# Kernel optimization log

Hardware: AMD Instinct MI355X
Metric: run time of the kernel (lower is better)

## Reference

```python
import jax, jax.numpy as jnp
import numpy as np
from jax import lax

B, N, T, H, E, V, F = 16, 5, 10, 512, 250, 30000, 2048  # N must be num_layers*num_dirs+1 = 5


def setup_inputs() -> dict:
    key = jax.random.key(0)
    ks = jax.random.split(key, 20)
    s = 0.05
    def rn(k, shp):
        return jax.random.normal(k, shp, jnp.float32) * s
    z = lambda n: jnp.zeros((n,), jnp.float32)
    return {
        "img": jax.random.normal(ks[0], (B, F), jnp.float32),
        "caps": jax.random.randint(ks[1], (B, N, T), 0, V, dtype=jnp.int32),
        "Wh1": rn(ks[2], (F, 2 * H)), "bh1": z(2 * H),
        "Wh2": rn(ks[3], (2 * H, H)), "bh2": z(H),
        "Wc1": rn(ks[4], (F, 2 * H)), "bc1": z(2 * H),
        "Wc2": rn(ks[5], (2 * H, H)), "bc2": z(H),
        "emb": rn(ks[6], (V, E)),
        "Wih0f": rn(ks[7], (E, 4 * H)), "Whh0f": rn(ks[8], (H, 4 * H)), "b0f": z(4 * H),
        "Wih0b": rn(ks[9], (E, 4 * H)), "Whh0b": rn(ks[10], (H, 4 * H)), "b0b": z(4 * H),
        "Wih1f": rn(ks[11], (2 * H, 4 * H)), "Whh1f": rn(ks[12], (H, 4 * H)), "b1f": z(4 * H),
        "Wih1b": rn(ks[13], (2 * H, 4 * H)), "Whh1b": rn(ks[14], (H, 4 * H)), "b1b": z(4 * H),
        "Wfc": rn(ks[15], (2 * H, V)), "bfc": z(V),
    }


def _lstm_dir(x, h0, c0, Wih, Whh, b, reverse):
    # x: [t, B, in]; PyTorch gate order i, f, g, o
    xs = x[::-1] if reverse else x
    xg = xs @ Wih + b  # precomputed input projection [t, B, 4H]
    def step(carry, xg_t):
        h, c = carry
        g = xg_t + h @ Whh
        i, f, gg, o = jnp.split(g, 4, axis=-1)
        c = jax.nn.sigmoid(f) * c + jax.nn.sigmoid(i) * jnp.tanh(gg)
        h = jax.nn.sigmoid(o) * jnp.tanh(c)
        return (h, c), h
    (hT, cT), hs = lax.scan(step, (h0, c0), xg)
    if reverse:
        hs = hs[::-1]
    return hs, hT, cT


def _bilstm2(x, h0, c0, p):
    # 2-layer bidirectional LSTM; state layout [l0_fwd, l0_bwd, l1_fwd, l1_bwd]
    of, hf0, cf0 = _lstm_dir(x, h0[0], c0[0], *p[0], False)
    ob, hb0, cb0 = _lstm_dir(x, h0[1], c0[1], *p[1], True)
    x1 = jnp.concatenate([of, ob], axis=-1)  # [t, B, 2H]
    o1f, hf1, cf1 = _lstm_dir(x1, h0[2], c0[2], *p[2], False)
    o1b, hb1, cb1 = _lstm_dir(x1, h0[3], c0[3], *p[3], True)
    out = jnp.concatenate([o1f, o1b], axis=-1)  # [t, B, 2H]
    hN = jnp.stack([hf0, hb0, hf1, hb1])
    cN = jnp.stack([cf0, cb0, cf1, cb1])
    return out, hN, cN


def _forward(img, caps, Wh1, bh1, Wh2, bh2, Wc1, bc1, Wc2, bc2, emb,
             Wih0f, Whh0f, b0f, Wih0b, Whh0b, b0b,
             Wih1f, Whh1f, b1f, Wih1b, Whh1b, b1b, Wfc, bfc):
    relu = jax.nn.relu
    h = relu(relu(img @ Wh1 + bh1) @ Wh2 + bh2)  # init_h MLP (dropout = identity in eval)
    c = relu(relu(img @ Wc1 + bc1) @ Wc2 + bc2)  # init_c MLP
    hs = jnp.broadcast_to(h[None], (N - 1, B, H))  # N-1 == 4 == num_layers*num_dirs
    cs = jnp.broadcast_to(c[None], (N - 1, B, H))
    seq = jnp.transpose(emb[caps], (1, 2, 0, 3))  # [N, T, B, E] caption-major prefixes
    p = ((Wih0f, Whh0f, b0f), (Wih0b, Whh0b, b0b),
         (Wih1f, Whh1f, b1f), (Wih1b, Whh1b, b1b))
    outs = None
    # Faithful reproduction of the original's redundant prefix recomputation:
    # at each outer step t, the LSTM is re-run on every caption's length-(t+1)
    # prefix, chaining (h, c) across captions; only the final step's outputs
    # survive, but the state chain depends on all prior iterations.
    for t in range(T):
        outs_t = []
        for n in range(N):
            o, hs, cs = _bilstm2(seq[n, :t + 1], hs, cs, p)
            outs_t.append(o)
        outs = outs_t
    out = jnp.stack(outs)  # [N, T, B, 2H]
    return out @ Wfc + bfc  # logits [N, T, B, V]


def reference(img, caps, Wh1, bh1, Wh2, bh2, Wc1, bc1, Wc2, bc2, emb,
              Wih0f, Whh0f, b0f, Wih0b, Whh0b, b0b,
              Wih1f, Whh1f, b1f, Wih1b, Whh1b, b1b, Wfc, bfc):
    return _forward(img, caps, Wh1, bh1, Wh2, bh2, Wc1, bc1, Wc2, bc2, emb,
                    Wih0f, Whh0f, b0f, Wih0b, Whh0b, b0b,
                    Wih1f, Whh1f, b1f, Wih1b, Whh1b, b1b, Wfc, bfc)
```

## Files before the change

kernel.cpp:

```cpp
#include <hip/hip_runtime.h>

typedef unsigned short u16;
typedef unsigned int   u32;
typedef unsigned long long u64;
typedef __attribute__((ext_vector_type(8))) short s8v;
typedef __attribute__((ext_vector_type(4))) float f4v;

#define DEVI __device__ __forceinline__

#define B_  16
#define N_  5
#define T_  10
#define H_  512
#define E_  250
#define V_  30000
#define F_  2048
#define FH  2048
#define H2  1024
#define NCOMP 128

__device__ u32   g_flag;
__device__ u32   g_slot[NCOMP];
__device__ __attribute__((aligned(64))) u16   g_H0[4*2*16*512];
__device__ __attribute__((aligned(64))) u16   g_H1[4*2*16*512];
__device__ __attribute__((aligned(64))) float g_cinit[16*512];
__device__ __attribute__((aligned(64))) u16   g_A1[2*2*16*1024];
__device__ __attribute__((aligned(64))) u16   g_X1[2*2*10*16*1024];
__device__ __attribute__((aligned(64))) u16   g_OUT1[2*800*1024];
__device__ __attribute__((aligned(64))) u16   g_TOK[800*256];

DEVI f4v MFMA(s8v a, s8v b, f4v c){ return __builtin_amdgcn_mfma_f32_16x16x32_bf16(a,b,c,0,0,0); }
DEVI float bf2f(u16 u){ union{u32 i; float f;} v; v.i = ((u32)u)<<16; return v.f; }
DEVI u16 f2bf(float f){ union{float f; u32 i;} v; v.f = f; u32 i = v.i + 0x7fffu + ((v.i>>16)&1u); return (u16)(i>>16); }
DEVI float sigm(float x){ return 1.0f/(1.0f+__expf(-x)); }
DEVI float tanhfast(float x){ float e = __expf(2.0f*x); return 1.0f - 2.0f/(e+1.0f); }

DEVI s8v ld16(const u16* p){ return *(const s8v*)p; }
DEVI s8v ld16u(const u16* p){ s8v a; __builtin_memcpy(&a, p, 16); return a; }

DEVI void ldc(s8v& d, const u16* p){
  asm volatile("global_load_dwordx4 %0, %1, off sc0 sc1" : "=v"(d) : "v"(p));
}
template<int N> DEVI void waitv(s8v& a){
  asm volatile("s_waitcnt vmcnt(%1)" : "+v"(a) : "n"(N));
}
template<int N> DEVI void waitv2(s8v& a, s8v& b){
  asm volatile("s_waitcnt vmcnt(%2)" : "+v"(a), "+v"(b) : "n"(N));
}

DEVI void st2c(u16* p, u16 v){
  asm volatile("global_store_short %0, %1, off sc0 sc1" :: "v"(p), "v"((u32)v) : "memory");
}

DEVI u16 ldw(const void* W, size_t idx, int f32){
  return f32 ? f2bf(((const float*)W)[idx]) : ((const u16*)W)[idx];
}
DEVI float ldwf(const void* W, size_t idx, int f32){
  return f32 ? ((const float*)W)[idx] : bf2f(((const u16*)W)[idx]);
}
DEVI s8v ldA8(const void* A, size_t idx, int f32){
  if(f32){
    const float* p = (const float*)A + idx;
    s8v a;
    #pragma unroll
    for(int j=0;j<8;++j) a[j] = (short)f2bf(p[j]);
    return a;
  }
  return ld16u((const u16*)A + idx);
}
DEVI s8v gatherBf(const void* W, int ld, int row0, int col, int f32){
  s8v r;
  #pragma unroll
  for(int j=0;j<8;++j) r[j] = (short)ldw(W, (size_t)(row0+j)*ld + col, f32);
  return r;
}

#define RPT4(M,b)  M(b) M((b)+1) M((b)+2) M((b)+3)
#define RPT8(M,b)  RPT4(M,b) RPT4(M,(b)+4)
#define RPT16(M,b) RPT8(M,b) RPT8(M,(b)+8)

__global__ __launch_bounds__(64) void k0(const void* img){
  int l = threadIdx.x;
  const u16* p = (const u16*)img;
  int bad = 0;
  #pragma unroll
  for(int i=0;i<4;++i){
    float v = bf2f(p[l + 64*i]);
    if(!(fabsf(v) <= 1e4f)) bad = 1;
  }
  unsigned long long mb = __ballot(bad);
  g_slot[l] = 0u; g_slot[l+64] = 0u;
  if(l==0){ g_flag = (mb != 0ull) ? 1u : 0u; }
}

__global__ __launch_bounds__(256) void k_tok(const int* caps, const void* emb){
  int f32 = (int)g_flag;
  int idx = blockIdx.x*256 + threadIdx.x;
  int bnr = idx>>8, e = idx&255;
  int tok = caps[bnr];
  u16 v = (e < E_) ? ldw(emb, (size_t)tok*E_ + e, f32) : (u16)0;
  g_TOK[idx] = v;
}

__global__ __launch_bounds__(256) void k1a(const void* img, const void* Wh1, const void* bh1,
                                           const void* Wc1, const void* bc1){
  int f32 = (int)g_flag;
  int w = threadIdx.x>>6, l = threadIdx.x&63, q = l>>4, c = l&15, m = l&15;
  int widx = blockIdx.x*4 + w;
  int which = widx>>6;
  int ct    = widx&63;
  const void* W    = which? Wc1 : Wh1;
  const void* bias = which? bc1 : bh1;
  int col = ct*16 + c;
  f4v acc = {0.f,0.f,0.f,0.f};
  for(int kc=0; kc<64; ++kc){
    s8v a = ldA8(img, (size_t)m*F_ + kc*32 + q*8, f32);
    s8v b = gatherBf(W, H2, kc*32+q*8, col, f32);
    acc = MFMA(a,b,acc);
  }
  float bi = ldwf(bias, col, f32);
  #pragma unroll
  for(int r=0;r<4;++r){
    float v = fmaxf(acc[r]+bi, 0.f);
    u16 hi = f2bf(v); u16 lo = f2bf(v - bf2f(hi));
    int rowb = q*4+r;
    g_A1[(size_t)(which*2+0)*B_*H2 + (size_t)rowb*H2 + col] = hi;
    g_A1[(size_t)(which*2+1)*B_*H2 + (size_t)rowb*H2 + col] = lo;
  }
}

__global__ __launch_bounds__(256) void k1b(const void* Wh2, const void* bh2,
                                           const void* Wc2, const void* bc2){
  int f32 = (int)g_flag;
  int w = threadIdx.x>>6, l = threadIdx.x&63, q = l>>4, c = l&15, m = l&15;
  int widx = blockIdx.x*4 + w;
  int which = widx>>5;
  int ct    = widx&31;
  const void* W    = which? Wc2 : Wh2;
  const void* bias = which? bc2 : bh2;
  const u16* Ab    = g_A1 + (size_t)which*2*B_*H2;
  int col = ct*16 + c;
  f4v acc = {0.f,0.f,0.f,0.f};
  for(int kc=0; kc<32; ++kc){
    s8v ah = ld16(Ab + (size_t)m*H2 + kc*32 + q*8);
    s8v al = ld16(Ab + (size_t)B_*H2 + (size_t)m*H2 + kc*32 + q*8);
    s8v b  = gatherBf(W, H_, kc*32+q*8, col, f32);
    acc = MFMA(ah,b,acc);
    acc = MFMA(al,b,acc);
  }
  float bi = ldwf(bias, col, f32);
  #pragma unroll
  for(int r=0;r<4;++r){
    float v = fmaxf(acc[r]+bi, 0.f);
    int rowb = q*4+r;
    if(which==0){
      u16 hi = f2bf(v); u16 lo = f2bf(v - bf2f(hi));
      #pragma unroll
      for(int dir=0; dir<2; ++dir){
        size_t base = (size_t)(dir*2+0)*16384;
        g_H0[base + 0*8192 + rowb*512 + col] = hi;  g_H0[base + 1*8192 + rowb*512 + col] = lo;
        g_H1[base + 0*8192 + rowb*512 + col] = hi;  g_H1[base + 1*8192 + rowb*512 + col] = lo;
      }
    } else {
      g_cinit[(size_t)rowb*H_ + col] = v;
    }
  }
}

DEVI void flag_publish(u32 ep){
  asm volatile("s_waitcnt vmcnt(0)" ::: "memory");
  __syncthreads();
  if(threadIdx.x==0)
    __hip_atomic_store(&g_slot[blockIdx.x], ep, __ATOMIC_RELAXED, __HIP_MEMORY_SCOPE_SYSTEM);
}
DEVI void flag_poll(u32 ep){
  int l = threadIdx.x & 63;
  for(;;){
    u32 a = __hip_atomic_load(&g_slot[l],    __ATOMIC_RELAXED, __HIP_MEMORY_SCOPE_SYSTEM);
    u32 b = __hip_atomic_load(&g_slot[l+64], __ATOMIC_RELAXED, __HIP_MEMORY_SCOPE_SYSTEM);
    if(__all((int)(a>=ep && b>=ep))) break;
    __builtin_amdgcn_s_sleep(1);
  }
  asm volatile("s_waitcnt vmcnt(0)" ::: "memory");
}

DEVI float gate_combine(f4v acc, float& cs, int l){
  int base = (l & 48) | (l & 3);
  int sel  = (l >> 2) & 3;
  float G[4];
  #pragma unroll
  for(int gg=0; gg<4; ++gg){
    int src = base | (gg<<2);
    float a0 = __shfl(acc[0], src, 64);
    float a1 = __shfl(acc[1], src, 64);
    float a2 = __shfl(acc[2], src, 64);
    float a3 = __shfl(acc[3], src, 64);
    float x = (sel&1)? a1 : a0;
    float y = (sel&1)? a3 : a2;
    G[gg] = (sel&2)? y : x;
  }
  float iG = sigm(G[0]);
  float fG = sigm(G[1]);
  float gG = tanhfast(G[2]);
  float oG = sigm(G[3]);
  cs = fG*cs + iG*gG;
  return oG * tanhfast(cs);
}

__global__ __launch_bounds__(128) void k2(const void* Wih0f, const void* Whh0f, const void* b0f,
                                          const void* Wih0b, const void* Whh0b, const void* b0b,
                                          const void* Wih1f, const void* Whh1f, const void* b1f,
                                          const void* Wih1b, const void* Whh1b, const void* b1b){
  __shared__ u16 sw[2*24576];
  int tid = threadIdx.x;
  int blk = blockIdx.x;
  int f32 = (int)g_flag;
  int wv  = tid>>6;
  int l   = tid&63;
  int q = l>>4, c = l&15, m = l&15;
  int dir = blk>>6; int blkd = blk&63;
  int hb  = blkd*8;
  int gc0 = (c>>2)*512 + hb + (c&3);
  int gc1 = gc0 + 4;
  int bo  = q*4 + (c>>2);
  int hc0 = hb + (c&3), hc1 = hc0 + 4;

  const void* Wih0 = dir? Wih0b : Wih0f;
  const void* Whh0 = dir? Whh0b : Whh0f;
  const void* b0   = dir? b0b   : b0f;
  const void* Wih1 = dir? Wih1b : Wih1f;
  const void* Whh1 = dir? Whh1b : Whh1f;
  const void* b1   = dir? b1b   : b1f;

  for(int tt=0; tt<2; ++tt){
    int gb = hb + tt*4;
    for(int ii=tid; ii<24576; ii+=128){
      int kc=ii>>9, rem=ii&511, cc=rem>>5, qq=(rem>>3)&3, j=ii&7;
      int gc = (cc>>2)*512 + gb + (cc&3);
      int rowk = kc*32+qq*8+j;
      sw[tt*24576+ii] = (rowk < H2) ? ldw(Wih1, (size_t)rowk*FH + gc, f32)
                                    : ldw(Whh1, (size_t)(rowk-H2)*FH + gc, f32);
    }
  }

  s8v w0a[16], w0b[16], wxa[8], wxb[8];
  float cA0=0.f, cA1=0.f, biasA0=0.f, biasA1=0.f;
  float cB0=0.f, cB1=0.f, biasB0=0.f, biasB1=0.f;
  if(wv==0){
    #pragma unroll
    for(int kc=0;kc<16;++kc){
      #pragma unroll
      for(int j=0;j<8;++j){
        int rowk = kc*32+q*8+j;
        w0a[kc][j] = (short)ldw(Whh0, (size_t)rowk*FH + gc0, f32);
        w0b[kc][j] = (short)ldw(Whh0, (size_t)rowk*FH + gc1, f32);
      }
    }
    #pragma unroll
    for(int kc=0;kc<8;++kc){
      #pragma unroll
      for(int j=0;j<8;++j){
        int rowk = kc*32+q*8+j;
        wxa[kc][j] = (rowk<E_)? (short)ldw(Wih0, (size_t)rowk*FH + gc0, f32) : (short)0;
        wxb[kc][j] = (rowk<E_)? (short)ldw(Wih0, (size_t)rowk*FH + gc1, f32) : (short)0;
      }
    }
    biasA0 = ldwf(b0, gc0, f32); biasA1 = ldwf(b0, gc1, f32);
    cA0 = g_cinit[(size_t)bo*H_ + hc0]; cA1 = g_cinit[(size_t)bo*H_ + hc1];
  } else {
    biasB0 = ldwf(b1, gc0, f32); biasB1 = ldwf(b1, gc1, f32);
    cB0 = g_cinit[(size_t)bo*H_ + hc0]; cB1 = g_cinit[(size_t)bo*H_ + hc1];
  }
  __syncthreads();

  u32 ep = 0;
  int p0 = 0, p1 = 0;
  for(int k=0; k<=50; ++k){
    int Lk = (k<50) ? (k/5 + 1) : 10;
    int Lp = (k==0) ? 0 : ((k-1)/5 + 1);
    int n0 = k - (k/5)*5;
    int km = k-1;
    int n1 = (k>0) ? (km - (km/5)*5) : 0;
    for(int s=0; s<Lk; ++s){
      if(wv==0){
        if(k<50){
          int row = dir ? (Lk-1-s) : s;
          const u16* er = g_TOK + ((size_t)(m*N_ + n0)*T_ + row)*256;
          const u16* Hr = g_H0 + (size_t)(dir*2 + p0)*16384;
          f4v A0 = {biasA0,biasA0,biasA0,biasA0};
          f4v A1 = {biasA1,biasA1,biasA1,biasA1};
          #pragma unroll
          for(int kc=0;kc<8;++kc){
            s8v a = ld16(er + kc*32 + q*8);
            A0 = MFMA(a, wxa[kc], A0); A1 = MFMA(a, wxb[kc], A1);
          }
          flag_poll(ep);
          s8v hst[16];
#define H0ISS(f) ldc(hst[(f)], Hr + (((f)&1)?8192u:0u) + (size_t)m*H_ + (((f)>>1)*32) + q*8);
#define H0STEP(f) { \
          waitv<(((f)<16)?15:(31-(f)))>(hst[(f)&15]); \
          A0 = MFMA(hst[(f)&15], w0a[(f)>>1], A0); \
          A1 = MFMA(hst[(f)&15], w0b[(f)>>1], A1); \
          if((f)+16<32) ldc(hst[(f)&15], Hr + (((f)&1)?8192u:0u) + (size_t)m*H_ + (((((f)+16))>>1)*32) + q*8); }
          RPT16(H0ISS,0)
          RPT16(H0STEP,0) RPT16(H0STEP,16)
          float hn0 = gate_combine(A0, cA0, l);
          float hn1 = gate_combine(A1, cA1, l);
          u16 h0h=f2bf(hn0), h0l=f2bf(hn0 - bf2f(h0h));
          u16 h1h=f2bf(hn1), h1l=f2bf(hn1 - bf2f(h1h));
          u16* Hw = g_H0 + (size_t)(dir*2 + (p0^1))*16384;
          st2c(Hw + (size_t)bo*H_ + hc0, h0h); st2c(Hw + 8192 + (size_t)bo*H_ + hc0, h0l);
          st2c(Hw + (size_t)bo*H_ + hc1, h1h); st2c(Hw + 8192 + (size_t)bo*H_ + hc1, h1l);
          u16* Xw = g_X1 + (size_t)(k&1)*327680;
          size_t xr = ((size_t)row*16 + bo)*H2 + dir*H_;
          st2c(Xw + xr + hc0, h0h); st2c(Xw + 163840 + xr + hc0, h0l);
          st2c(Xw + xr + hc1, h1h); st2c(Xw + 163840 + xr + hc1, h1l);
          p0 ^= 1;
        }
      } else {
        if(k>0 && s<Lp){
          int row = dir ? (Lp-1-s) : s;
          const u16* Xr  = g_X1 + (size_t)(km&1)*327680 + ((size_t)row*16)*H2;
          const u16* Xr2 = Xr + 163840;
          const u16* Hr1 = g_H1 + (size_t)(dir*2 + p1)*16384;
          f4v A0 = {biasB0,biasB0,biasB0,biasB0};
          f4v A1 = {biasB1,biasB1,biasB1,biasB1};
          s8v sh[12], sl[12];
          if(s==0) flag_poll(ep);
#define XISS(kc) { ldc(sh[(kc)], Xr + (size_t)m*H2 + ((kc)*32) + q*8); \
                   ldc(sl[(kc)], Xr2 + (size_t)m*H2 + ((kc)*32) + q*8); }
#define XSTEP(kc) { \
          waitv2<(((kc)<20)?22:(62-2*(kc)))>(sh[(kc)%12], sl[(kc)%12]); \
          s8v bf0 = ld16(sw + (kc)*512 + c*32 + q*8); \
          s8v bf1 = ld16(sw + 24576 + (kc)*512 + c*32 + q*8); \
          A0 = MFMA(sh[(kc)%12], bf0, A0); A0 = MFMA(sl[(kc)%12], bf0, A0); \
          A1 = MFMA(sh[(kc)%12], bf1, A1); A1 = MFMA(sl[(kc)%12], bf1, A1); \
          if((kc)+12<32){ ldc(sh[(kc)%12], Xr + (size_t)m*H2 + (((kc)+12)*32) + q*8); \
                          ldc(sl[(kc)%12], Xr2 + (size_t)m*H2 + (((kc)+12)*32) + q*8); } }
          RPT8(XISS,0) RPT4(XISS,8)
          RPT16(XSTEP,0) RPT16(XSTEP,16)
          if(s>0) flag_poll(ep);
#define H1ISS(h) { ldc(sh[(h)], Hr1 + (size_t)m*H_ + ((h)*32) + q*8); \
                   ldc(sl[(h)], Hr1 + 8192 + (size_t)m*H_ + ((h)*32) + q*8); }
#define H1STEP(h) { \
          waitv2<(((h)<4)?22:(30-2*(h)))>(sh[(h)%12], sl[(h)%12]); \
          s8v bf0 = ld16(sw + (32+(h))*512 + c*32 + q*8); \
          s8v bf1 = ld16(sw + 24576 + (32+(h))*512 + c*32 + q*8); \
          A0 = MFMA(sh[(h)%12], bf0, A0); A0 = MFMA(sl[(h)%12], bf0, A0); \
          A1 = MFMA(sh[(h)%12], bf1, A1); A1 = MFMA(sl[(h)%12], bf1, A1); \
          if((h)+12<16){ ldc(sh[(h)%12], Hr1 + (size_t)m*H_ + (((h)+12)*32) + q*8); \
                         ldc(sl[(h)%12], Hr1 + 8192 + (size_t)m*H_ + (((h)+12)*32) + q*8); } }
          RPT8(H1ISS,0) RPT4(H1ISS,8)
          RPT16(H1STEP,0)
          float hn0 = gate_combine(A0, cB0, l);
          float hn1 = gate_combine(A1, cB1, l);
          u16 h0h=f2bf(hn0), h0l=f2bf(hn0 - bf2f(h0h));
          u16 h1h=f2bf(hn1), h1l=f2bf(hn1 - bf2f(h1h));
          u16* Hw = g_H1 + (size_t)(dir*2 + (p1^1))*16384;
          st2c(Hw + (size_t)bo*H_ + hc0, h0h); st2c(Hw + 8192 + (size_t)bo*H_ + hc0, h0l);
          st2c(Hw + (size_t)bo*H_ + hc1, h1h); st2c(Hw + 8192 + (size_t)bo*H_ + hc1, h1l);
          size_t orow = (size_t)(n1*10 + row)*16 + bo;
          st2c(g_OUT1 + orow*H2 + dir*H_ + hc0, h0h);
          st2c(g_OUT1 + (size_t)800*H2 + orow*H2 + dir*H_ + hc0, h0l);
          st2c(g_OUT1 + orow*H2 + dir*H_ + hc1, h1h);
          st2c(g_OUT1 + (size_t)800*H2 + orow*H2 + dir*H_ + hc1, h1l);
          p1 ^= 1;
        }
      }
      flag_publish(ep+1);
      ++ep;
    }
  }
}

__global__ __launch_bounds__(256,1) void k3(const void* Wfc, const void* bfc, void* out){
  int f32 = (int)g_flag;
  int w = threadIdx.x>>6, l = threadIdx.x&63, q = l>>4, c = l&15, m = l&15;
  int ct = blockIdx.x*4 + w;
  if(ct >= 1875) return;
  int col = ct*16 + c;
  s8v bfr[32];
  #pragma unroll
  for(int kc=0; kc<32; ++kc){
    #pragma unroll
    for(int j=0;j<8;++j) bfr[kc][j] = (short)ldw(Wfc, (size_t)(kc*32+q*8+j)*V_ + col, f32);
  }
  float bi = ldwf(bfc, col, f32);
  for(int rt=0; rt<50; ++rt){
    f4v acc = {0.f,0.f,0.f,0.f};
    const u16* Ah = g_OUT1 + (size_t)(rt*16 + m)*H2;
    const u16* Al = Ah + (size_t)800*H2;
    #pragma unroll
    for(int kc=0; kc<32; ++kc){
      acc = MFMA(ld16(Ah + kc*32 + q*8), bfr[kc], acc);
      acc = MFMA(ld16(Al + kc*32 + q*8), bfr[kc], acc);
    }
    if(f32){
      float* o = (float*)out;
      #pragma unroll
      for(int r=0;r<4;++r) o[(size_t)(rt*16 + q*4 + r)*V_ + col] = acc[r] + bi;
    } else {
      u16* o = (u16*)out;
      #pragma unroll
      for(int r=0;r<4;++r) o[(size_t)(rt*16 + q*4 + r)*V_ + col] = f2bf(acc[r] + bi);
    }
  }
}

extern "C" void kernel_launch(void* const* d_in, const int* in_sizes, int n_in,
                              void* d_out, int out_size, void* d_ws, size_t ws_size,
                              hipStream_t stream){
  (void)in_sizes; (void)n_in; (void)out_size; (void)d_ws; (void)ws_size;
  const void* img  = d_in[0];
  const int*  caps = (const int*)d_in[1];
  const void* Wh1=d_in[2],  *bh1=d_in[3];
  const void* Wh2=d_in[4],  *bh2=d_in[5];
  const void* Wc1=d_in[6],  *bc1=d_in[7];
  const void* Wc2=d_in[8],  *bc2=d_in[9];
  const void* emb=d_in[10];
  const void* Wih0f=d_in[11], *Whh0f=d_in[12], *b0f=d_in[13];
  const void* Wih0b=d_in[14], *Whh0b=d_in[15], *b0b=d_in[16];
  const void* Wih1f=d_in[17], *Whh1f=d_in[18], *b1f=d_in[19];
  const void* Wih1b=d_in[20], *Whh1b=d_in[21], *b1b=d_in[22];
  const void* Wfc=d_in[23],  *bfc=d_in[24];

  hipLaunchKernelGGL(k0,    dim3(1),     dim3(64),  0, stream, img);
  hipLaunchKernelGGL(k_tok, dim3(800),   dim3(256), 0, stream, caps, emb);
  hipLaunchKernelGGL(k1a,   dim3(32),    dim3(256), 0, stream, img, Wh1, bh1, Wc1, bc1);
  hipLaunchKernelGGL(k1b,   dim3(16),    dim3(256), 0, stream, Wh2, bh2, Wc2, bc2);
  hipLaunchKernelGGL(k2,    dim3(NCOMP), dim3(128), 0, stream,
                     Wih0f, Whh0f, b0f, Wih0b, Whh0b, b0b,
                     Wih1f, Whh1f, b1f, Wih1b, Whh1b, b1b);
  hipLaunchKernelGGL(k3,    dim3(469),   dim3(256), 0, stream, Wfc, bfc, d_out);
}
```

Baseline: 3.612 ms.

## Decouple layer-0 and layer-1 LSTM waves with separate per-layer progress flags

```diff
diff --git a/kernel.cpp b/kernel.cpp
--- a/kernel.cpp
+++ b/kernel.cpp
@@ -20,12 +20,13 @@
 #define NCOMP 128
 
 __device__ u32   g_flag;
-__device__ u32   g_slot[NCOMP];
+__device__ u32   g_slot0[NCOMP];
+__device__ u32   g_slot1[NCOMP];
 __device__ __attribute__((aligned(64))) u16   g_H0[4*2*16*512];
 __device__ __attribute__((aligned(64))) u16   g_H1[4*2*16*512];
 __device__ __attribute__((aligned(64))) float g_cinit[16*512];
 __device__ __attribute__((aligned(64))) u16   g_A1[2*2*16*1024];
-__device__ __attribute__((aligned(64))) u16   g_X1[2*2*10*16*1024];
+__device__ __attribute__((aligned(64))) u16   g_X1[4*2*10*16*1024];
 __device__ __attribute__((aligned(64))) u16   g_OUT1[2*800*1024];
 __device__ __attribute__((aligned(64))) u16   g_TOK[800*256];
 
@@ -79,6 +80,31 @@
 #define RPT8(M,b)  RPT4(M,b) RPT4(M,(b)+4)
 #define RPT16(M,b) RPT8(M,b) RPT8(M,(b)+8)
 
+DEVI void publish_slot(u32* slot, u32 val){
+  asm volatile("s_waitcnt vmcnt(0)" ::: "memory");
+  if((threadIdx.x & 63)==0)
+    __hip_atomic_store(slot, val, __ATOMIC_RELAXED, __HIP_MEMORY_SCOPE_SYSTEM);
+}
+DEVI void poll_n64(u32* base, u32 tgt){
+  int l = threadIdx.x & 63;
+  for(;;){
+    u32 a = __hip_atomic_load(&base[l], __ATOMIC_RELAXED, __HIP_MEMORY_SCOPE_SYSTEM);
+    if(__all((int)(a>=tgt))) break;
+    __builtin_amdgcn_s_sleep(1);
+  }
+  asm volatile("s_waitcnt vmcnt(0)" ::: "memory");
+}
+DEVI void poll_n128(u32* base, u32 tgt){
+  int l = threadIdx.x & 63;
+  for(;;){
+    u32 a = __hip_atomic_load(&base[l],    __ATOMIC_RELAXED, __HIP_MEMORY_SCOPE_SYSTEM);
+    u32 b = __hip_atomic_load(&base[l+64], __ATOMIC_RELAXED, __HIP_MEMORY_SCOPE_SYSTEM);
+    if(__all((int)(a>=tgt && b>=tgt))) break;
+    __builtin_amdgcn_s_sleep(1);
+  }
+  asm volatile("s_waitcnt vmcnt(0)" ::: "memory");
+}
+
 __global__ __launch_bounds__(64) void k0(const void* img){
   int l = threadIdx.x;
   const u16* p = (const u16*)img;
@@ -89,7 +115,8 @@
     if(!(fabsf(v) <= 1e4f)) bad = 1;
   }
   unsigned long long mb = __ballot(bad);
-  g_slot[l] = 0u; g_slot[l+64] = 0u;
+  g_slot0[l] = 0u; g_slot0[l+64] = 0u;
+  g_slot1[l] = 0u; g_slot1[l+64] = 0u;
   if(l==0){ g_flag = (mb != 0ull) ? 1u : 0u; }
 }
 
@@ -167,23 +194,6 @@
   }
 }
 
-DEVI void flag_publish(u32 ep){
-  asm volatile("s_waitcnt vmcnt(0)" ::: "memory");
-  __syncthreads();
-  if(threadIdx.x==0)
-    __hip_atomic_store(&g_slot[blockIdx.x], ep, __ATOMIC_RELAXED, __HIP_MEMORY_SCOPE_SYSTEM);
-}
-DEVI void flag_poll(u32 ep){
-  int l = threadIdx.x & 63;
-  for(;;){
-    u32 a = __hip_atomic_load(&g_slot[l],    __ATOMIC_RELAXED, __HIP_MEMORY_SCOPE_SYSTEM);
-    u32 b = __hip_atomic_load(&g_slot[l+64], __ATOMIC_RELAXED, __HIP_MEMORY_SCOPE_SYSTEM);
-    if(__all((int)(a>=ep && b>=ep))) break;
-    __builtin_amdgcn_s_sleep(1);
-  }
-  asm volatile("s_waitcnt vmcnt(0)" ::: "memory");
-}
-
 DEVI float gate_combine(f4v acc, float& cs, int l){
   int base = (l & 48) | (l & 3);
   int sel  = (l >> 2) & 3;
@@ -273,102 +283,105 @@
   }
   __syncthreads();
 
-  u32 ep = 0;
-  int p0 = 0, p1 = 0;
-  for(int k=0; k<=50; ++k){
-    int Lk = (k<50) ? (k/5 + 1) : 10;
-    int Lp = (k==0) ? 0 : ((k-1)/5 + 1);
-    int n0 = k - (k/5)*5;
-    int km = k-1;
-    int n1 = (k>0) ? (km - (km/5)*5) : 0;
-    for(int s=0; s<Lk; ++s){
-      if(wv==0){
-        if(k<50){
-          int row = dir ? (Lk-1-s) : s;
-          const u16* er = g_TOK + ((size_t)(m*N_ + n0)*T_ + row)*256;
-          const u16* Hr = g_H0 + (size_t)(dir*2 + p0)*16384;
-          f4v A0 = {biasA0,biasA0,biasA0,biasA0};
-          f4v A1 = {biasA1,biasA1,biasA1,biasA1};
-          #pragma unroll
-          for(int kc=0;kc<8;++kc){
-            s8v a = ld16(er + kc*32 + q*8);
-            A0 = MFMA(a, wxa[kc], A0); A1 = MFMA(a, wxb[kc], A1);
-          }
-          flag_poll(ep);
-          s8v hst[16];
+  if(wv==0){
+    u32 i0 = 0; int p0 = 0;
+    for(int k=0; k<50; ++k){
+      int Lk = k/5 + 1; int n0 = k - (k/5)*5;
+      if(k>=4){
+        u32 need = 0;
+        for(int j=0;j<k-3;++j) need += (u32)(j/5+1);
+        poll_n128(g_slot1, need);
+      }
+      for(int s=0; s<Lk; ++s){
+        int row = dir ? (Lk-1-s) : s;
+        const u16* er = g_TOK + ((size_t)(m*N_ + n0)*T_ + row)*256;
+        const u16* Hr = g_H0 + (size_t)(dir*2 + p0)*16384;
+        f4v A0 = {biasA0,biasA0,biasA0,biasA0};
+        f4v A1 = {biasA1,biasA1,biasA1,biasA1};
+        #pragma unroll
+        for(int kc=0;kc<8;++kc){
+          s8v a = ld16(er + kc*32 + q*8);
+          A0 = MFMA(a, wxa[kc], A0); A1 = MFMA(a, wxb[kc], A1);
+        }
+        poll_n64(g_slot0 + dir*64, i0);
+        s8v hst[16];
 #define H0ISS(f) ldc(hst[(f)], Hr + (((f)&1)?8192u:0u) + (size_t)m*H_ + (((f)>>1)*32) + q*8);
 #define H0STEP(f) { \
-          waitv<(((f)<16)?15:(31-(f)))>(hst[(f)&15]); \
-          A0 = MFMA(hst[(f)&15], w0a[(f)>>1], A0); \
-          A1 = MFMA(hst[(f)&15], w0b[(f)>>1], A1); \
-          if((f)+16<32) ldc(hst[(f)&15], Hr + (((f)&1)?8192u:0u) + (size_t)m*H_ + (((((f)+16))>>1)*32) + q*8); }
-          RPT16(H0ISS,0)
-          RPT16(H0STEP,0) RPT16(H0STEP,16)
-          float hn0 = gate_combine(A0, cA0, l);
-          float hn1 = gate_combine(A1, cA1, l);
-          u16 h0h=f2bf(hn0), h0l=f2bf(hn0 - bf2f(h0h));
-          u16 h1h=f2bf(hn1), h1l=f2bf(hn1 - bf2f(h1h));
-          u16* Hw = g_H0 + (size_t)(dir*2 + (p0^1))*16384;
-          st2c(Hw + (size_t)bo*H_ + hc0, h0h); st2c(Hw + 8192 + (size_t)bo*H_ + hc0, h0l);
-          st2c(Hw + (size_t)bo*H_ + hc1, h1h); st2c(Hw + 8192 + (size_t)bo*H_ + hc1, h1l);
-          u16* Xw = g_X1 + (size_t)(k&1)*327680;
-          size_t xr = ((size_t)row*16 + bo)*H2 + dir*H_;
-          st2c(Xw + xr + hc0, h0h); st2c(Xw + 163840 + xr + hc0, h0l);
-          st2c(Xw + xr + hc1, h1h); st2c(Xw + 163840 + xr + hc1, h1l);
-          p0 ^= 1;
-        }
-      } else {
-        if(k>0 && s<Lp){
-          int row = dir ? (Lp-1-s) : s;
-          const u16* Xr  = g_X1 + (size_t)(km&1)*327680 + ((size_t)row*16)*H2;
-          const u16* Xr2 = Xr + 163840;
-          const u16* Hr1 = g_H1 + (size_t)(dir*2 + p1)*16384;
-          f4v A0 = {biasB0,biasB0,biasB0,biasB0};
-          f4v A1 = {biasB1,biasB1,biasB1,biasB1};
-          s8v sh[12], sl[12];
-          if(s==0) flag_poll(ep);
+        waitv<(((f)<16)?15:(31-(f)))>(hst[(f)&15]); \
+        A0 = MFMA(hst[(f)&15], w0a[(f)>>1], A0); \
+        A1 = MFMA(hst[(f)&15], w0b[(f)>>1], A1); \
+        if((f)+16<32) ldc(hst[(f)&15], Hr + (((f)&1)?8192u:0u) + (size_t)m*H_ + (((((f)+16))>>1)*32) + q*8); }
+        RPT16(H0ISS,0)
+        RPT16(H0STEP,0) RPT16(H0STEP,16)
+        float hn0 = gate_combine(A0, cA0, l);
+        float hn1 = gate_combine(A1, cA1, l);
+        u16 h0h=f2bf(hn0), h0l=f2bf(hn0 - bf2f(h0h));
+        u16 h1h=f2bf(hn1), h1l=f2bf(hn1 - bf2f(h1h));
+        u16* Hw = g_H0 + (size_t)(dir*2 + (p0^1))*16384;
+        st2c(Hw + (size_t)bo*H_ + hc0, h0h); st2c(Hw + 8192 + (size_t)bo*H_ + hc0, h0l);
+        st2c(Hw + (size_t)bo*H_ + hc1, h1h); st2c(Hw + 8192 + (size_t)bo*H_ + hc1, h1l);
+        u16* Xw = g_X1 + (size_t)(k&3)*327680;
+        size_t xr = ((size_t)row*16 + bo)*H2 + dir*H_;
+        st2c(Xw + xr + hc0, h0h); st2c(Xw + 163840 + xr + hc0, h0l);
+        st2c(Xw + xr + hc1, h1h); st2c(Xw + 163840 + xr + hc1, h1l);
+        publish_slot(&g_slot0[blk], i0+1);
+        ++i0; p0 ^= 1;
+      }
+    }
+  } else {
+    u32 i1 = 0, Sc = 0; int p1 = 0;
+    for(int cl=0; cl<50; ++cl){
+      int Lc = cl/5 + 1; int n1 = cl - (cl/5)*5;
+      poll_n128(g_slot0, Sc + (u32)Lc);
+      for(int s=0; s<Lc; ++s){
+        int row = dir ? (Lc-1-s) : s;
+        const u16* Xr  = g_X1 + (size_t)(cl&3)*327680 + ((size_t)row*16)*H2;
+        const u16* Xr2 = Xr + 163840;
+        const u16* Hr1 = g_H1 + (size_t)(dir*2 + p1)*16384;
+        f4v A0 = {biasB0,biasB0,biasB0,biasB0};
+        f4v A1 = {biasB1,biasB1,biasB1,biasB1};
+        s8v sh[12], sl[12];
 #define XISS(kc) { ldc(sh[(kc)], Xr + (size_t)m*H2 + ((kc)*32) + q*8); \
                    ldc(sl[(kc)], Xr2 + (size_t)m*H2 + ((kc)*32) + q*8); }
 #define XSTEP(kc) { \
-          waitv2<(((kc)<20)?22:(62-2*(kc)))>(sh[(kc)%12], sl[(kc)%12]); \
-          s8v bf0 = ld16(sw + (kc)*512 + c*32 + q*8); \
-          s8v bf1 = ld16(sw + 24576 + (kc)*512 + c*32 + q*8); \
-          A0 = MFMA(sh[(kc)%12], bf0, A0); A0 = MFMA(sl[(kc)%12], bf0, A0); \
-          A1 = MFMA(sh[(kc)%12], bf1, A1); A1 = MFMA(sl[(kc)%12], bf1, A1); \
-          if((kc)+12<32){ ldc(sh[(kc)%12], Xr + (size_t)m*H2 + (((kc)+12)*32) + q*8); \
-                          ldc(sl[(kc)%12], Xr2 + (size_t)m*H2 + (((kc)+12)*32) + q*8); } }
-          RPT8(XISS,0) RPT4(XISS,8)
-          RPT16(XSTEP,0) RPT16(XSTEP,16)
-          if(s>0) flag_poll(ep);
+        waitv2<(((kc)<20)?22:(62-2*(kc)))>(sh[(kc)%12], sl[(kc)%12]); \
+        s8v bf0 = ld16(sw + (kc)*512 + c*32 + q*8); \
+        s8v bf1 = ld16(sw + 24576 + (kc)*512 + c*32 + q*8); \
+        A0 = MFMA(sh[(kc)%12], bf0, A0); A0 = MFMA(sl[(kc)%12], bf0, A0); \
+        A1 = MFMA(sh[(kc)%12], bf1, A1); A1 = MFMA(sl[(kc)%12], bf1, A1); \
+        if((kc)+12<32){ ldc(sh[(kc)%12], Xr + (size_t)m*H2 + (((kc)+12)*32) + q*8); \
+                        ldc(sl[(kc)%12], Xr2 + (size_t)m*H2 + (((kc)+12)*32) + q*8); } }
+        RPT8(XISS,0) RPT4(XISS,8)
+        RPT16(XSTEP,0) RPT16(XSTEP,16)
+        poll_n64(g_slot1 + dir*64, i1);
 #define H1ISS(h) { ldc(sh[(h)], Hr1 + (size_t)m*H_ + ((h)*32) + q*8); \
                    ldc(sl[(h)], Hr1 + 8192 + (size_t)m*H_ + ((h)*32) + q*8); }
 #define H1STEP(h) { \
-          waitv2<(((h)<4)?22:(30-2*(h)))>(sh[(h)%12], sl[(h)%12]); \
-          s8v bf0 = ld16(sw + (32+(h))*512 + c*32 + q*8); \
-          s8v bf1 = ld16(sw + 24576 + (32+(h))*512 + c*32 + q*8); \
-          A0 = MFMA(sh[(h)%12], bf0, A0); A0 = MFMA(sl[(h)%12], bf0, A0); \
-          A1 = MFMA(sh[(h)%12], bf1, A1); A1 = MFMA(sl[(h)%12], bf1, A1); \
-          if((h)+12<16){ ldc(sh[(h)%12], Hr1 + (size_t)m*H_ + (((h)+12)*32) + q*8); \
-                         ldc(sl[(h)%12], Hr1 + 8192 + (size_t)m*H_ + (((h)+12)*32) + q*8); } }
-          RPT8(H1ISS,0) RPT4(H1ISS,8)
-          RPT16(H1STEP,0)
-          float hn0 = gate_combine(A0, cB0, l);
-          float hn1 = gate_combine(A1, cB1, l);
-          u16 h0h=f2bf(hn0), h0l=f2bf(hn0 - bf2f(h0h));
-          u16 h1h=f2bf(hn1), h1l=f2bf(hn1 - bf2f(h1h));
-          u16* Hw = g_H1 + (size_t)(dir*2 + (p1^1))*16384;
-          st2c(Hw + (size_t)bo*H_ + hc0, h0h); st2c(Hw + 8192 + (size_t)bo*H_ + hc0, h0l);
-          st2c(Hw + (size_t)bo*H_ + hc1, h1h); st2c(Hw + 8192 + (size_t)bo*H_ + hc1, h1l);
-          size_t orow = (size_t)(n1*10 + row)*16 + bo;
-          st2c(g_OUT1 + orow*H2 + dir*H_ + hc0, h0h);
-          st2c(g_OUT1 + (size_t)800*H2 + orow*H2 + dir*H_ + hc0, h0l);
-          st2c(g_OUT1 + orow*H2 + dir*H_ + hc1, h1h);
-          st2c(g_OUT1 + (size_t)800*H2 + orow*H2 + dir*H_ + hc1, h1l);
-          p1 ^= 1;
-        }
-      }
-      flag_publish(ep+1);
-      ++ep;
+        waitv2<(((h)<4)?22:(30-2*(h)))>(sh[(h)%12], sl[(h)%12]); \
+        s8v bf0 = ld16(sw + (32+(h))*512 + c*32 + q*8); \
+        s8v bf1 = ld16(sw + 24576 + (32+(h))*512 + c*32 + q*8); \
+        A0 = MFMA(sh[(h)%12], bf0, A0); A0 = MFMA(sl[(h)%12], bf0, A0); \
+        A1 = MFMA(sh[(h)%12], bf1, A1); A1 = MFMA(sl[(h)%12], bf1, A1); \
+        if((h)+12<16){ ldc(sh[(h)%12], Hr1 + (size_t)m*H_ + (((h)+12)*32) + q*8); \
+                       ldc(sl[(h)%12], Hr1 + 8192 + (size_t)m*H_ + (((h)+12)*32) + q*8); } }
+        RPT8(H1ISS,0) RPT4(H1ISS,8)
+        RPT16(H1STEP,0)
+        float hn0 = gate_combine(A0, cB0, l);
+        float hn1 = gate_combine(A1, cB1, l);
+        u16 h0h=f2bf(hn0), h0l=f2bf(hn0 - bf2f(h0h));
+        u16 h1h=f2bf(hn1), h1l=f2bf(hn1 - bf2f(h1h));
+        u16* Hw = g_H1 + (size_t)(dir*2 + (p1^1))*16384;
+        st2c(Hw + (size_t)bo*H_ + hc0, h0h); st2c(Hw + 8192 + (size_t)bo*H_ + hc0, h0l);
+        st2c(Hw + (size_t)bo*H_ + hc1, h1h); st2c(Hw + 8192 + (size_t)bo*H_ + hc1, h1l);
+        size_t orow = (size_t)(n1*10 + row)*16 + bo;
+        st2c(g_OUT1 + orow*H2 + dir*H_ + hc0, h0h);
+        st2c(g_OUT1 + (size_t)800*H2 + orow*H2 + dir*H_ + hc0, h0l);
+        st2c(g_OUT1 + orow*H2 + dir*H_ + hc1, h1h);
+        st2c(g_OUT1 + (size_t)800*H2 + orow*H2 + dir*H_ + hc1, h1l);
+        publish_slot(&g_slot1[blk], i1+1);
+        ++i1; p1 ^= 1;
+      }
+      Sc += (u32)Lc;
     }
   }
 }
```

Result: no change. 3.682 ms (+1.9%).

## Coalesce LSTM hidden-state stores via LDS transpose into 16-byte writes

Applied to the files above, without the earlier changes.

```diff
diff --git a/kernel.cpp b/kernel.cpp
--- a/kernel.cpp
+++ b/kernel.cpp
@@ -50,6 +50,9 @@
 
 DEVI void st2c(u16* p, u16 v){
   asm volatile("global_store_short %0, %1, off sc0 sc1" :: "v"(p), "v"((u32)v) : "memory");
+}
+DEVI void st16c(u16* p, s8v v){
+  asm volatile("global_store_dwordx4 %0, %1, off sc0 sc1" :: "v"(p), "v"(v) : "memory");
 }
 
 DEVI u16 ldw(const void* W, size_t idx, int f32){
@@ -113,6 +116,7 @@
   const void* bias = which? bc1 : bh1;
   int col = ct*16 + c;
   f4v acc = {0.f,0.f,0.f,0.f};
+  #pragma unroll 4
   for(int kc=0; kc<64; ++kc){
     s8v a = ldA8(img, (size_t)m*F_ + kc*32 + q*8, f32);
     s8v b = gatherBf(W, H2, kc*32+q*8, col, f32);
@@ -141,6 +145,7 @@
   const u16* Ab    = g_A1 + (size_t)which*2*B_*H2;
   int col = ct*16 + c;
   f4v acc = {0.f,0.f,0.f,0.f};
+  #pragma unroll 4
   for(int kc=0; kc<32; ++kc){
     s8v ah = ld16(Ab + (size_t)m*H2 + kc*32 + q*8);
     s8v al = ld16(Ab + (size_t)B_*H2 + (size_t)m*H2 + kc*32 + q*8);
@@ -212,18 +217,21 @@
                                           const void* Wih1f, const void* Whh1f, const void* b1f,
                                           const void* Wih1b, const void* Whh1b, const void* b1b){
   __shared__ u16 sw[2*24576];
+  __shared__ __attribute__((aligned(16))) u32 tr0[128];
+  __shared__ __attribute__((aligned(16))) u32 tr1[128];
   int tid = threadIdx.x;
   int blk = blockIdx.x;
   int f32 = (int)g_flag;
   int wv  = tid>>6;
   int l   = tid&63;
   int q = l>>4, c = l&15, m = l&15;
+  int l8 = l*8;
   int dir = blk>>6; int blkd = blk&63;
   int hb  = blkd*8;
-  int gc0 = (c>>2)*512 + hb + (c&3);
-  int gc1 = gc0 + 4;
+  int gc0 = (c>>2)*512 + hb + 2*(c&3);
+  int gc1 = gc0 + 1;
   int bo  = q*4 + (c>>2);
-  int hc0 = hb + (c&3), hc1 = hc0 + 4;
+  int hc0 = hb + 2*(c&3), hc1 = hc0 + 1;
 
   const void* Wih0 = dir? Wih0b : Wih0f;
   const void* Whh0 = dir? Whh0b : Whh0f;
@@ -233,10 +241,12 @@
   const void* b1   = dir? b1b   : b1f;
 
   for(int tt=0; tt<2; ++tt){
-    int gb = hb + tt*4;
     for(int ii=tid; ii<24576; ii+=128){
-      int kc=ii>>9, rem=ii&511, cc=rem>>5, qq=(rem>>3)&3, j=ii&7;
-      int gc = (cc>>2)*512 + gb + (cc&3);
+      int kc = ii>>9;
+      int lane = (ii>>3)&63;
+      int j  = ii&7;
+      int cc = lane&15, qq = lane>>4;
+      int gc = (cc>>2)*512 + hb + 2*(cc&3) + tt;
       int rowk = kc*32+qq*8+j;
       sw[tt*24576+ii] = (rowk < H2) ? ldw(Wih1, (size_t)rowk*FH + gc, f32)
                                     : ldw(Whh1, (size_t)(rowk-H2)*FH + gc, f32);
@@ -308,13 +318,17 @@
           float hn1 = gate_combine(A1, cA1, l);
           u16 h0h=f2bf(hn0), h0l=f2bf(hn0 - bf2f(h0h));
           u16 h1h=f2bf(hn1), h1l=f2bf(hn1 - bf2f(h1h));
-          u16* Hw = g_H0 + (size_t)(dir*2 + (p0^1))*16384;
-          st2c(Hw + (size_t)bo*H_ + hc0, h0h); st2c(Hw + 8192 + (size_t)bo*H_ + hc0, h0l);
-          st2c(Hw + (size_t)bo*H_ + hc1, h1h); st2c(Hw + 8192 + (size_t)bo*H_ + hc1, h1l);
-          u16* Xw = g_X1 + (size_t)(k&1)*327680;
-          size_t xr = ((size_t)row*16 + bo)*H2 + dir*H_;
-          st2c(Xw + xr + hc0, h0h); st2c(Xw + 163840 + xr + hc0, h0l);
-          st2c(Xw + xr + hc1, h1h); st2c(Xw + 163840 + xr + hc1, h1l);
+          tr0[(c&3) + bo*4]      = (u32)h0h | ((u32)h1h<<16);
+          tr0[64 + (c&3) + bo*4] = (u32)h0l | ((u32)h1l<<16);
+          asm volatile("s_waitcnt lgkmcnt(0)" ::: "memory");
+          if(l<32){
+            s8v v = *(const s8v*)&tr0[l*4];
+            int pl2 = l>>4, rw = l&15;
+            u16* Hw = g_H0 + (size_t)(dir*2 + (p0^1))*16384;
+            st16c(Hw + pl2*8192 + rw*512 + hb, v);
+            u16* Xw = g_X1 + (size_t)(k&1)*327680;
+            st16c(Xw + (size_t)pl2*163840 + ((size_t)row*16 + rw)*H2 + dir*H_ + hb, v);
+          }
           p0 ^= 1;
         }
       } else {
@@ -331,8 +345,8 @@
                    ldc(sl[(kc)], Xr2 + (size_t)m*H2 + ((kc)*32) + q*8); }
 #define XSTEP(kc) { \
           waitv2<(((kc)<20)?22:(62-2*(kc)))>(sh[(kc)%12], sl[(kc)%12]); \
-          s8v bf0 = ld16(sw + (kc)*512 + c*32 + q*8); \
-          s8v bf1 = ld16(sw + 24576 + (kc)*512 + c*32 + q*8); \
+          s8v bf0 = ld16(sw + (kc)*512 + l8); \
+          s8v bf1 = ld16(sw + 24576 + (kc)*512 + l8); \
           A0 = MFMA(sh[(kc)%12], bf0, A0); A0 = MFMA(sl[(kc)%12], bf0, A0); \
           A1 = MFMA(sh[(kc)%12], bf1, A1); A1 = MFMA(sl[(kc)%12], bf1, A1); \
           if((kc)+12<32){ ldc(sh[(kc)%12], Xr + (size_t)m*H2 + (((kc)+12)*32) + q*8); \
@@ -344,8 +358,8 @@
                    ldc(sl[(h)], Hr1 + 8192 + (size_t)m*H_ + ((h)*32) + q*8); }
 #define H1STEP(h) { \
           waitv2<(((h)<4)?22:(30-2*(h)))>(sh[(h)%12], sl[(h)%12]); \
-          s8v bf0 = ld16(sw + (32+(h))*512 + c*32 + q*8); \
-          s8v bf1 = ld16(sw + 24576 + (32+(h))*512 + c*32 + q*8); \
+          s8v bf0 = ld16(sw + (32+(h))*512 + l8); \
+          s8v bf1 = ld16(sw + 24576 + (32+(h))*512 + l8); \
           A0 = MFMA(sh[(h)%12], bf0, A0); A0 = MFMA(sl[(h)%12], bf0, A0); \
           A1 = MFMA(sh[(h)%12], bf1, A1); A1 = MFMA(sl[(h)%12], bf1, A1); \
           if((h)+12<16){ ldc(sh[(h)%12], Hr1 + (size_t)m*H_ + (((h)+12)*32) + q*8); \
@@ -356,14 +370,17 @@
           float hn1 = gate_combine(A1, cB1, l);
           u16 h0h=f2bf(hn0), h0l=f2bf(hn0 - bf2f(h0h));
           u16 h1h=f2bf(hn1), h1l=f2bf(hn1 - bf2f(h1h));
-          u16* Hw = g_H1 + (size_t)(dir*2 + (p1^1))*16384;
-          st2c(Hw + (size_t)bo*H_ + hc0, h0h); st2c(Hw + 8192 + (size_t)bo*H_ + hc0, h0l);
-          st2c(Hw + (size_t)bo*H_ + hc1, h1h); st2c(Hw + 8192 + (size_t)bo*H_ + hc1, h1l);
-          size_t orow = (size_t)(n1*10 + row)*16 + bo;
-          st2c(g_OUT1 + orow*H2 + dir*H_ + hc0, h0h);
-          st2c(g_OUT1 + (size_t)800*H2 + orow*H2 + dir*H_ + hc0, h0l);
-          st2c(g_OUT1 + orow*H2 + dir*H_ + hc1, h1h);
-          st2c(g_OUT1 + (size_t)800*H2 + orow*H2 + dir*H_ + hc1, h1l);
+          tr1[(c&3) + bo*4]      = (u32)h0h | ((u32)h1h<<16);
+          tr1[64 + (c&3) + bo*4] = (u32)h0l | ((u32)h1l<<16);
+          asm volatile("s_waitcnt lgkmcnt(0)" ::: "memory");
+          if(l<32){
+            s8v v = *(const s8v*)&tr1[l*4];
+            int pl2 = l>>4, rw = l&15;
+            u16* Hw = g_H1 + (size_t)(dir*2 + (p1^1))*16384;
+            st16c(Hw + pl2*8192 + rw*512 + hb, v);
+            size_t orow = (size_t)(n1*10 + row)*16 + rw;
+            st16c(g_OUT1 + (size_t)pl2*819200 + orow*H2 + dir*H_ + hb, v);
+          }
           p1 ^= 1;
         }
       }
```

After: 3.621 ms. No clear change (+0.2%).
